# Optimization experiments

Measured on AMD Instinct MI355X. Metric: run time of the kernel, lower is better.

## Reference

```python
import jax, jax.numpy as jnp
import numpy as np
from jax import lax

DIM = 192
D_STATE = 16
D_CONV = 4
EXPAND = 2
DT_RANK = 12  # ceil(192/16)
D_INNER = EXPAND * DIM
MLP_HID = int(DIM * 4.0)
B_, T_, H_, W_ = 2, 8, 24, 24


def _mamba_params(key, prefix):
    ks = jax.random.split(key, 6)
    s = 0.02
    return {
        prefix + "_in_proj_w": jax.random.normal(ks[0], (2 * D_INNER, DIM)) * s,
        prefix + "_conv_w": jax.random.normal(ks[1], (D_INNER, D_CONV)) * s,
        prefix + "_conv_b": jnp.zeros((D_INNER,)),
        prefix + "_x_proj_w": jax.random.normal(ks[2], (DT_RANK + 2 * D_STATE, D_INNER)) * s,
        prefix + "_dt_proj_w": jax.random.normal(ks[3], (D_INNER, DT_RANK)) * s,
        prefix + "_dt_proj_b": jax.random.uniform(ks[4], (D_INNER,), minval=-4.0, maxval=-2.0),
        prefix + "_A_log": jnp.log(jnp.broadcast_to(jnp.arange(1, D_STATE + 1, dtype=jnp.float32), (D_INNER, D_STATE))),
        prefix + "_D": jnp.ones((D_INNER,)),
        prefix + "_out_proj_w": jax.random.normal(ks[5], (DIM, D_INNER)) * s,
    }


def setup_inputs() -> dict:
    key = jax.random.key(0)
    ks = jax.random.split(key, 8)
    s = 0.02
    inp = {"x_in": jax.random.normal(ks[0], (B_, T_, DIM, H_, W_), dtype=jnp.float32)}
    inp["norm1_w"] = jnp.ones((DIM,)); inp["norm1_b"] = jnp.zeros((DIM,))
    inp.update(_mamba_params(ks[1], "s"))
    inp.update(_mamba_params(ks[2], "t"))
    inp["fusion_w"] = jax.random.normal(ks[3], (DIM, 2 * DIM)) * s
    inp["fusion_b"] = jnp.zeros((DIM,))
    inp["norm2_w"] = jnp.ones((DIM,)); inp["norm2_b"] = jnp.zeros((DIM,))
    inp["mlp_w1"] = jax.random.normal(ks[4], (MLP_HID, DIM)) * s
    inp["mlp_b1"] = jnp.zeros((MLP_HID,))
    inp["mlp_w2"] = jax.random.normal(ks[5], (DIM, MLP_HID)) * s
    inp["mlp_b2"] = jnp.zeros((DIM,))
    return inp


def _layer_norm(x, w, b, eps=1e-5):
    m = jnp.mean(x, axis=-1, keepdims=True)
    v = jnp.mean(jnp.square(x - m), axis=-1, keepdims=True)
    return (x - m) * lax.rsqrt(v + eps) * w + b


def _selective_scan(u, delta, A, Bm, Cm, Dp):
    # u, delta: [b,L,d]; A: [d,n]; Bm, Cm: [b,L,n]; Dp: [d]
    dA = jnp.exp(delta[..., None] * A)                       # [b,L,d,n]
    dBu = (delta * u)[..., None] * Bm[:, :, None, :]         # [b,L,d,n]

    def step(h, inp):
        dA_t, dBu_t, C_t = inp                               # [b,d,n],[b,d,n],[b,n]
        h = dA_t * h + dBu_t
        y = jnp.einsum('bdn,bn->bd', h, C_t)
        return h, y

    h0 = jnp.zeros((u.shape[0],) + A.shape, dtype=u.dtype)
    xs = (jnp.moveaxis(dA, 1, 0), jnp.moveaxis(dBu, 1, 0), jnp.moveaxis(Cm, 1, 0))
    _, ys = lax.scan(step, h0, xs)                           # [L,b,d]
    return jnp.moveaxis(ys, 0, 1) + u * Dp


def _mamba(x, in_proj_w, conv_w, conv_b, x_proj_w, dt_proj_w, dt_proj_b, A_log, Dp, out_proj_w):
    # x: [b, L, d_model]
    xz = x @ in_proj_w.T                                     # [b,L,2*d_inner]
    xm, z = jnp.split(xz, 2, axis=-1)
    # causal depthwise conv1d (kernel D_CONV, left-padded)
    xc = jnp.pad(xm, ((0, 0), (D_CONV - 1, 0), (0, 0)))
    kernel = conv_w.T[:, None, :]                            # [W=4, I=1, O=d_inner]
    xm = lax.conv_general_dilated(xc, kernel, (1,), 'VALID',
                                  dimension_numbers=('NWC', 'WIO', 'NWC'),
                                  feature_group_count=D_INNER) + conv_b
    xm = jax.nn.silu(xm)
    dbc = xm @ x_proj_w.T                                    # [b,L,dt_rank+2n]
    dt, Bm, Cm = jnp.split(dbc, [DT_RANK, DT_RANK + D_STATE], axis=-1)
    delta = jax.nn.softplus(dt @ dt_proj_w.T + dt_proj_b)    # [b,L,d_inner]
    A = -jnp.exp(A_log)
    y = _selective_scan(xm, delta, A, Bm, Cm, Dp)
    y = y * jax.nn.silu(z)
    return y @ out_proj_w.T


def reference(x_in, norm1_w, norm1_b,
              s_in_proj_w, s_conv_w, s_conv_b, s_x_proj_w, s_dt_proj_w, s_dt_proj_b, s_A_log, s_D, s_out_proj_w,
              t_in_proj_w, t_conv_w, t_conv_b, t_x_proj_w, t_dt_proj_w, t_dt_proj_b, t_A_log, t_D, t_out_proj_w,
              fusion_w, fusion_b, norm2_w, norm2_b, mlp_w1, mlp_b1, mlp_w2, mlp_b2):
    B, T, C, H, W = x_in.shape
    N = H * W
    x = jnp.transpose(x_in, (0, 1, 3, 4, 2)).reshape(B, T, N, C)
    shortcut = x
    xn = _layer_norm(x, norm1_w, norm1_b)
    out_s = _mamba(xn.reshape(B * T, N, C), s_in_proj_w, s_conv_w, s_conv_b, s_x_proj_w,
                   s_dt_proj_w, s_dt_proj_b, s_A_log, s_D, s_out_proj_w).reshape(B, T, N, C)
    x_t = jnp.transpose(xn, (0, 2, 1, 3)).reshape(B * N, T, C)
    out_t = _mamba(x_t, t_in_proj_w, t_conv_w, t_conv_b, t_x_proj_w,
                   t_dt_proj_w, t_dt_proj_b, t_A_log, t_D, t_out_proj_w)
    out_t = jnp.transpose(out_t.reshape(B, N, T, C), (0, 2, 1, 3))
    fused = jnp.concatenate([out_s, out_t], axis=-1)
    x = shortcut + (fused @ fusion_w.T + fusion_b)
    h = _layer_norm(x, norm2_w, norm2_b)
    h = jax.nn.gelu(h @ mlp_w1.T + mlp_b1, approximate=False) @ mlp_w2.T + mlp_b2
    x = x + h
    return jnp.transpose(x.reshape(B, T, H, W, C), (0, 1, 4, 2, 3))
```

## Files before the change

### kernel.cpp

```cpp
#include <hip/hip_runtime.h>
#include <hip/hip_bf16.h>

#define NB 2
#define NT 8
#define NHW 576
#define NC 192
#define DIN 384
#define NSTATE 16
#define MTOK 9216
#define MLPH 768
#define SCH 36
#define CLEN 16
#define NSEQ_S 16
#define L2E 1.44269504088896f
#define LN2 0.69314718055994f

typedef const __hip_bfloat16* bf16p;
typedef __hip_bfloat16 bf16;

typedef __attribute__((ext_vector_type(8))) short frag_ab;
typedef __attribute__((ext_vector_type(4))) float frag_cd;

__device__ __forceinline__ float b2f(__hip_bfloat16 x) { return __bfloat162float(x); }
__device__ __forceinline__ bf16 f2b(float x) { return __float2bfloat16(x); }

__device__ __forceinline__ bool is_f32(const unsigned* __restrict__ n1w) {
    return n1w[0] == 0x3F800000u;
}

__device__ __forceinline__ float ldv(const void* p, long long i, bool f32) {
    return f32 ? ((const float*)p)[i] : b2f(((const bf16*)p)[i]);
}

__device__ __forceinline__ float siluf(float x) { return x / (1.f + expf(-x)); }
__device__ __forceinline__ float softplus_fast(float x) {
    float e = exp2f(-fabsf(x) * L2E);
    return fmaxf(x, 0.f) + log2f(1.f + e) * LN2;
}
__device__ __forceinline__ float geluf(float x) { return 0.5f * x * (1.f + erff(x * 0.7071067811865476f)); }

__device__ __forceinline__ float wave_sum(float v) {
#pragma unroll
    for (int o = 32; o > 0; o >>= 1) v += __shfl_xor(v, o, 64);
    return v;
}

__global__ __launch_bounds__(256) void ln1_kernel(const void* x_in, const void* w, const void* b,
                                                  bf16* __restrict__ xn,
                                                  bf16* __restrict__ xnt,
                                                  bf16* __restrict__ shortcut,
                                                  const unsigned* __restrict__ n1w) {
    bool f32 = is_f32(n1w);
    int bt = blockIdx.x / 9;
    int hw0 = (blockIdx.x % 9) * 64;
    int bb = bt >> 3, tt = bt & 7;
    int t = threadIdx.x, l = t & 63, wv = t >> 6;
    __shared__ bf16 lv[192 * 66];
    __shared__ float psum[4][64], psq[4][64];
    __shared__ float smean[64], srstd[64];
    __shared__ float swl[192], sbl[192];
    for (int i = t; i < 192; i += 256) { swl[i] = ldv(w, i, f32); sbl[i] = ldv(b, i, f32); }
    float s = 0.f, q = 0.f;
#pragma unroll 4
    for (int cg = 0; cg < 48; cg++) {
        int c = wv * 48 + cg;
        float v = ldv(x_in, (long long)(bt * NC + c) * NHW + hw0 + l, f32);
        lv[c * 66 + l] = f2b(v);
        s += v; q += v * v;
    }
    psum[wv][l] = s; psq[wv][l] = q;
    __syncthreads();
    if (t < 64) {
        float ss = psum[0][t] + psum[1][t] + psum[2][t] + psum[3][t];
        float qq = psq[0][t] + psq[1][t] + psq[2][t] + psq[3][t];
        float mean = ss * (1.f / NC);
        float var = qq * (1.f / NC) - mean * mean;
        smean[t] = mean;
        srstd[t] = rsqrtf(var + 1e-5f);
    }
    __syncthreads();
    for (int jj = 0; jj < 64; jj++) {
        if (t < 192) {
            int n = hw0 + jj;
            long long m = (long long)(bt * NHW + n) * NC + t;
            long long mt = ((long long)(bb * NHW + n) * NT + tt) * NC + t;
            bf16 raw = lv[t * 66 + jj];
            float v = b2f(raw);
            bf16 xv = f2b((v - smean[jj]) * srstd[jj] * swl[t] + sbl[t]);
            shortcut[m] = raw;
            xn[m] = xv;
            xnt[mt] = xv;
        }
    }
}

__global__ __launch_bounds__(64) void ln2_kernel(const float* __restrict__ x, const void* w, const void* b,
                                                 bf16* __restrict__ out,
                                                 const unsigned* __restrict__ n1w) {
    bool f32 = is_f32(n1w);
    int m = blockIdx.x;
    int lane = threadIdx.x;
    float v[3];
#pragma unroll
    for (int r = 0; r < 3; r++) v[r] = x[m * NC + lane + r * 64];
    float s = wave_sum(v[0] + v[1] + v[2]);
    float mean = s * (1.f / NC);
    float q = 0.f;
#pragma unroll
    for (int r = 0; r < 3; r++) { float d = v[r] - mean; q += d * d; }
    q = wave_sum(q);
    float rstd = rsqrtf(q * (1.f / NC) + 1e-5f);
#pragma unroll
    for (int r = 0; r < 3; r++) {
        int c = lane + r * 64;
        out[m * NC + c] = f2b((v[r] - mean) * rstd * ldv(w, c, f32) + ldv(b, c, f32));
    }
}

__device__ __forceinline__ void store_val(float* p, float v) { *p = v; }
__device__ __forceinline__ void store_val(bf16* p, float v) { *p = f2b(v); }
__device__ __forceinline__ float load_val(const float* p) { return *p; }
__device__ __forceinline__ float load_val(const bf16* p) { return b2f(*p); }

__device__ __forceinline__ long long fmode_rowbase(int FMODE, int gm, int N) {
    if (FMODE == 0) return (long long)gm * N;
    if (FMODE == 1) return (long long)gm * 384;
    int b = gm / (NHW * NT);
    int rr = gm % (NHW * NT);
    int n = rr / NT;
    int t = rr % NT;
    int ms = (b * NT + t) * NHW + n;
    return (long long)ms * 384 + 192;
}

#define LDSTR 40
template <int ACT, int FMODE, bool BCHK, typename OutT, typename AddT>
__global__ __launch_bounds__(256) void gemm_mfma(bf16p A, const void* W, const void* bias,
                                                 const AddT* __restrict__ addsrc,
                                                 OutT* __restrict__ out,
                                                 int M, int N, int K,
                                                 const unsigned* __restrict__ n1w) {
    bool f32 = is_f32(n1w);
    __shared__ bf16 lds_a[128 * LDSTR];
    __shared__ bf16 lds_b[64 * LDSTR];
    int tid = threadIdx.x;
    int m0 = blockIdx.y * 128, n0 = blockIdx.x * 64;
    int wv = tid >> 6;
    int lane = tid & 63;
    int lr = lane & 15;
    int quad = lane >> 4;
    int wm = (wv >> 1) * 64;
    int wn = (wv & 1) * 32;

    frag_cd acc[4][2] = {};

    for (int kc = 0; kc < K; kc += 32) {
#pragma unroll
        for (int p = 0; p < 2; p++) {
            int idx = p * 256 + tid;
            int row = idx >> 2;
            int kcol = (idx & 3) * 8;
            *(uint4*)&lds_a[row * LDSTR + kcol] =
                *(const uint4*)&A[(size_t)(m0 + row) * K + kc + kcol];
        }
        {
            int row = tid >> 2;
            int kcol = (tid & 3) * 8;
            bool ok = !BCHK || (n0 + row) < N;
            if (f32) {
                const float* Wf = (const float*)W;
#pragma unroll
                for (int j = 0; j < 8; j++)
                    lds_b[row * LDSTR + kcol + j] =
                        ok ? f2b(Wf[(size_t)(n0 + row) * K + kc + kcol + j]) : f2b(0.f);
            } else {
                uint4 z = {0, 0, 0, 0};
                *(uint4*)&lds_b[row * LDSTR + kcol] =
                    ok ? *(const uint4*)&((const bf16*)W)[(size_t)(n0 + row) * K + kc + kcol] : z;
            }
        }
        __syncthreads();

        frag_ab af[4], bfr[2];
#pragma unroll
        for (int tm = 0; tm < 4; tm++)
            af[tm] = *(const frag_ab*)&lds_a[(wm + tm * 16 + lr) * LDSTR + quad * 8];
#pragma unroll
        for (int tn = 0; tn < 2; tn++)
            bfr[tn] = *(const frag_ab*)&lds_b[(wn + tn * 16 + lr) * LDSTR + quad * 8];
#pragma unroll
        for (int tm = 0; tm < 4; tm++)
#pragma unroll
            for (int tn = 0; tn < 2; tn++)
                acc[tm][tn] = __builtin_amdgcn_mfma_f32_16x16x32_bf16(
                    af[tm], bfr[tn], acc[tm][tn], 0, 0, 0);
        __syncthreads();
    }

#pragma unroll
    for (int tm = 0; tm < 4; tm++) {
#pragma unroll
        for (int r = 0; r < 4; r++) {
            int gm = m0 + wm + tm * 16 + quad * 4 + r;
            long long rowbase = fmode_rowbase(FMODE, gm, N);
#pragma unroll
            for (int tn = 0; tn < 2; tn++) {
                int gn = n0 + wn + tn * 16 + lr;
                if (BCHK && gn >= N) continue;
                float v = acc[tm][tn][r];
                if (bias) v += ldv(bias, gn, f32);
                if (ACT == 1) v = geluf(v);
                if (addsrc) v += load_val(&addsrc[(long long)gm * N + gn]);
                store_val(&out[rowbase + gn], v);
            }
        }
    }
}

template <bool BCHK, int WOFF, typename OutT>
__global__ __launch_bounds__(256) void gemm_dual(bf16p A0, bf16p A1,
                                                 const void* W0, const void* W1,
                                                 OutT* __restrict__ out0,
                                                 OutT* __restrict__ out1,
                                                 int M, int N, int K,
                                                 const unsigned* __restrict__ n1w) {
    bool f32 = is_f32(n1w);
    __shared__ bf16 lds_a[128 * LDSTR];
    __shared__ bf16 lds_b[64 * LDSTR];
    int tid = threadIdx.x;
    bool br0 = blockIdx.y < (unsigned)(M / 128);
    int m0 = (br0 ? blockIdx.y : blockIdx.y - M / 128) * 128;
    int n0 = blockIdx.x * 64;
    bf16p A = br0 ? A0 : A1;
    const void* W = br0 ? W0 : W1;
    OutT* out = br0 ? out0 : out1;
    int wv = tid >> 6;
    int lane = tid & 63;
    int lr = lane & 15;
    int quad = lane >> 4;
    int wm = (wv >> 1) * 64;
    int wn = (wv & 1) * 32;

    frag_cd acc[4][2] = {};

    for (int kc = 0; kc < K; kc += 32) {
#pragma unroll
        for (int p = 0; p < 2; p++) {
            int idx = p * 256 + tid;
            int row = idx >> 2;
            int kcol = (idx & 3) * 8;
            *(uint4*)&lds_a[row * LDSTR + kcol] =
                *(const uint4*)&A[(size_t)(m0 + row) * K + kc + kcol];
        }
        {
            int row = tid >> 2;
            int kcol = (tid & 3) * 8;
            bool ok = !BCHK || (n0 + row) < N;
            size_t wrow = (size_t)(WOFF + n0 + row);
            if (f32) {
                const float* Wf = (const float*)W;
#pragma unroll
                for (int j = 0; j < 8; j++)
                    lds_b[row * LDSTR + kcol + j] =
                        ok ? f2b(Wf[wrow * K + kc + kcol + j]) : f2b(0.f);
            } else {
                uint4 z = {0, 0, 0, 0};
                *(uint4*)&lds_b[row * LDSTR + kcol] =
                    ok ? *(const uint4*)&((const bf16*)W)[wrow * K + kc + kcol] : z;
            }
        }
        __syncthreads();

        frag_ab af[4], bfr[2];
#pragma unroll
        for (int tm = 0; tm < 4; tm++)
            af[tm] = *(const frag_ab*)&lds_a[(wm + tm * 16 + lr) * LDSTR + quad * 8];
#pragma unroll
        for (int tn = 0; tn < 2; tn++)
            bfr[tn] = *(const frag_ab*)&lds_b[(wn + tn * 16 + lr) * LDSTR + quad * 8];
#pragma unroll
        for (int tm = 0; tm < 4; tm++)
#pragma unroll
            for (int tn = 0; tn < 2; tn++)
                acc[tm][tn] = __builtin_amdgcn_mfma_f32_16x16x32_bf16(
                    af[tm], bfr[tn], acc[tm][tn], 0, 0, 0);
        __syncthreads();
    }

#pragma unroll
    for (int tm = 0; tm < 4; tm++) {
#pragma unroll
        for (int r = 0; r < 4; r++) {
            int gm = m0 + wm + tm * 16 + quad * 4 + r;
#pragma unroll
            for (int tn = 0; tn < 2; tn++) {
                int gn = n0 + wn + tn * 16 + lr;
                if (BCHK && gn >= N) continue;
                store_val(&out[(long long)gm * N + gn], acc[tm][tn][r]);
            }
        }
    }
}

__global__ __launch_bounds__(256) void gemm_outproj_dual(bf16p ys_s, bf16p ys_t,
                                                         const void* w_s, const void* w_t,
                                                         bf16* __restrict__ fused,
                                                         const unsigned* __restrict__ n1w) {
    bool f32 = is_f32(n1w);
    __shared__ bf16 lds_a[128 * LDSTR];
    __shared__ bf16 lds_b[64 * LDSTR];
    int tid = threadIdx.x;
    bool spatial = blockIdx.y < (MTOK / 128);
    int m0 = (spatial ? blockIdx.y : blockIdx.y - MTOK / 128) * 128;
    int n0 = blockIdx.x * 64;
    bf16p A = spatial ? ys_s : ys_t;
    const void* W = spatial ? w_s : w_t;
    const int K = DIN;
    int wv = tid >> 6;
    int lane = tid & 63;
    int lr = lane & 15;
    int quad = lane >> 4;
    int wm = (wv >> 1) * 64;
    int wn = (wv & 1) * 32;

    frag_cd acc[4][2] = {};

    for (int kc = 0; kc < K; kc += 32) {
#pragma unroll
        for (int p = 0; p < 2; p++) {
            int idx = p * 256 + tid;
            int row = idx >> 2;
            int kcol = (idx & 3) * 8;
            *(uint4*)&lds_a[row * LDSTR + kcol] =
                *(const uint4*)&A[(size_t)(m0 + row) * K + kc + kcol];
        }
        {
            int row = tid >> 2;
            int kcol = (tid & 3) * 8;
            if (f32) {
                const float* Wf = (const float*)W;
#pragma unroll
                for (int j = 0; j < 8; j++)
                    lds_b[row * LDSTR + kcol + j] =
                        f2b(Wf[(size_t)(n0 + row) * K + kc + kcol + j]);
            } else {
                *(uint4*)&lds_b[row * LDSTR + kcol] =
                    *(const uint4*)&((const bf16*)W)[(size_t)(n0 + row) * K + kc + kcol];
            }
        }
        __syncthreads();

        frag_ab af[4], bfr[2];
#pragma unroll
        for (int tm = 0; tm < 4; tm++)
            af[tm] = *(const frag_ab*)&lds_a[(wm + tm * 16 + lr) * LDSTR + quad * 8];
#pragma unroll
        for (int tn = 0; tn < 2; tn++)
            bfr[tn] = *(const frag_ab*)&lds_b[(wn + tn * 16 + lr) * LDSTR + quad * 8];
#pragma unroll
        for (int tm = 0; tm < 4; tm++)
#pragma unroll
            for (int tn = 0; tn < 2; tn++)
                acc[tm][tn] = __builtin_amdgcn_mfma_f32_16x16x32_bf16(
                    af[tm], bfr[tn], acc[tm][tn], 0, 0, 0);
        __syncthreads();
    }

#pragma unroll
    for (int tm = 0; tm < 4; tm++) {
#pragma unroll
        for (int r = 0; r < 4; r++) {
            int gm = m0 + wm + tm * 16 + quad * 4 + r;
            long long rowbase = fmode_rowbase(spatial ? 1 : 2, gm, NC);
#pragma unroll
            for (int tn = 0; tn < 2; tn++) {
                int gn = n0 + wn + tn * 16 + lr;
                fused[rowbase + gn] = f2b(acc[tm][tn][r]);
            }
        }
    }
}

#define TOTEL (MTOK * DIN)
__global__ __launch_bounds__(256) void conv_dual(bf16p xs, const void* cw_s, const void* cb_s,
                                                 bf16p xt, const void* cw_t, const void* cb_t,
                                                 bf16* __restrict__ xm_s,
                                                 bf16* __restrict__ xm_t,
                                                 const unsigned* __restrict__ n1w) {
    bool f32 = is_f32(n1w);
    long long gidx = (long long)blockIdx.x * blockDim.x + threadIdx.x;
    bool sp = gidx < TOTEL;
    long long idx = sp ? gidx : gidx - TOTEL;
    bf16p x = sp ? xs : xt;
    const void* cw = sp ? cw_s : cw_t;
    const void* cb = sp ? cb_s : cb_t;
    bf16* xm = sp ? xm_s : xm_t;
    int L = sp ? NHW : NT;
    int d = (int)(idx % DIN);
    long long rem = idx / DIN;
    int l = (int)(rem % L);
    long long seq = rem / L;
    float s = ldv(cb, d, f32);
#pragma unroll
    for (int k = 0; k < 4; k++) {
        int ll = l - 3 + k;
        if (ll >= 0) s += ldv(cw, d * 4 + k, f32) * b2f(x[(seq * L + ll) * DIN + d]);
    }
    xm[(seq * L + l) * DIN + d] = f2b(siluf(s));
}

template <int TL>
__global__ __launch_bounds__(128) void scan_kernel(bf16p xm,
                                                   const float* __restrict__ dbc,
                                                   bf16* __restrict__ zy,
                                                   const void* dtw, const void* dtb,
                                                   const void* A_log, const void* Dv,
                                                   const unsigned* __restrict__ n1w) {
    bool f32 = is_f32(n1w);
    int seq = blockIdx.x / 3;
    int d = (blockIdx.x % 3) * 128 + threadIdx.x;
    int row0 = seq * TL;
    __shared__ float sdbc[TL * 44];
    for (int i = threadIdx.x; i < TL * 44; i += 128)
        sdbc[i] = dbc[(long long)row0 * 44 + i];
    bf16 um[TL], zm[TL];
#pragma unroll
    for (int t = 0; t < TL; t++) {
        um[t] = xm[(long long)(row0 + t) * DIN + d];
        zm[t] = zy[(long long)(row0 + t) * DIN + d];
    }
    float A2[NSTATE], h[NSTATE];
#pragma unroll
    for (int n = 0; n < NSTATE; n++) {
        A2[n] = -expf(ldv(A_log, d * NSTATE + n, f32)) * L2E;
        h[n] = 0.f;
    }
    float wdt[12];
#pragma unroll
    for (int r = 0; r < 12; r++) wdt[r] = ldv(dtw, d * 12 + r, f32);
    float bdt = ldv(dtb, d, f32);
    float Dd = ldv(Dv, d, f32);
    __syncthreads();
#pragma unroll
    for (int t = 0; t < TL; t++) {
        const float* dr = &sdbc[t * 44];
        float s = bdt;
#pragma unroll
        for (int r = 0; r < 12; r++) s += dr[r] * wdt[r];
        float dv = softplus_fast(s);
        float uv = b2f(um[t]);
        float du = dv * uv;
        float y = 0.f;
#pragma unroll
        for (int n = 0; n < NSTATE; n++) {
            float dA = exp2f(dv * A2[n]);
            h[n] = h[n] * dA + du * dr[12 + n];
            y += h[n] * dr[28 + n];
        }
        y += uv * Dd;
        zy[(long long)(row0 + t) * DIN + d] = f2b(y * siluf(b2f(zm[t])));
    }
}

__global__ __launch_bounds__(256) void scan1_kernel(bf16p xm,
                                                    const float* __restrict__ dbc,
                                                    const void* dtw, const void* dtb,
                                                    const void* A_log,
                                                    bf16* __restrict__ hfin,
                                                    float* __restrict__ dsumb,
                                                    const unsigned* __restrict__ n1w) {
    bool f32 = is_f32(n1w);
    int bid = blockIdx.x;
    int part = bid % 3;
    int ch = (bid / 3) % SCH;
    int seq = bid / (3 * SCH);
    int tid = threadIdx.x;
    int wave = tid >> 6;
    int lane = tid & 63;
    int dl = lane & 31;
    int nh = lane >> 5;
    int d = part * 128 + wave * 32 + dl;
    int nbase = nh * 8;
    int row0 = seq * NHW + ch * CLEN;
    __shared__ float sdbc[CLEN * 44];
    for (int i = tid; i < CLEN * 44; i += 256)
        sdbc[i] = dbc[(long long)row0 * 44 + i];
    bf16 um[CLEN];
#pragma unroll
    for (int t = 0; t < CLEN; t++)
        um[t] = xm[(long long)(row0 + t) * DIN + d];
    float A2[8], h[8];
#pragma unroll
    for (int j = 0; j < 8; j++) {
        A2[j] = -expf(ldv(A_log, d * NSTATE + nbase + j, f32)) * L2E;
        h[j] = 0.f;
    }
    float wdt[12];
#pragma unroll
    for (int r = 0; r < 12; r++) wdt[r] = ldv(dtw, d * 12 + r, f32);
    float bdt = ldv(dtb, d, f32);
    float dsum = 0.f;
    __syncthreads();
#pragma unroll
    for (int t = 0; t < CLEN; t++) {
        const float* dr = &sdbc[t * 44];
        float s = bdt;
#pragma unroll
        for (int r = 0; r < 12; r++) s += dr[r] * wdt[r];
        float dv = softplus_fast(s);
        dsum += dv;
        float du = dv * b2f(um[t]);
#pragma unroll
        for (int j = 0; j < 8; j++) {
            float dA = exp2f(dv * A2[j]);
            h[j] = h[j] * dA + du * dr[12 + nbase + j];
        }
    }
    long long base = (((long long)seq * SCH + ch) * DIN + d) * NSTATE + nbase;
#pragma unroll
    for (int j = 0; j < 8; j++) hfin[base + j] = f2b(h[j]);
    if (nh == 0) dsumb[((long long)seq * SCH + ch) * DIN + d] = dsum;
}

__global__ __launch_bounds__(256) void scan2_kernel(bf16* __restrict__ hfin,
                                                    const float* __restrict__ dsumb,
                                                    const void* A_log,
                                                    const unsigned* __restrict__ n1w) {
    bool f32 = is_f32(n1w);
    int e = blockIdx.x * blockDim.x + threadIdx.x;
    int seq = e / (DIN * NSTATE);
    int dn = e % (DIN * NSTATE);
    int d = dn >> 4;
    float A2 = -expf(ldv(A_log, dn, f32)) * L2E;
    float hrun = 0.f;
    for (int ch = 0; ch < SCH; ch++) {
        long long cidx = (long long)seq * SCH + ch;
        float p = exp2f(dsumb[cidx * DIN + d] * A2);
        long long idx = cidx * (DIN * NSTATE) + dn;
        float hf = b2f(hfin[idx]);
        hfin[idx] = f2b(hrun);
        hrun = p * hrun + hf;
    }
}

__global__ __launch_bounds__(256) void scan3_kernel(bf16p xm,
                                                    const float* __restrict__ dbc,
                                                    bf16* __restrict__ zy,
                                                    const void* dtw, const void* dtb,
                                                    const void* A_log, const void* Dv,
                                                    const bf16* __restrict__ hinit,
                                                    const unsigned* __restrict__ n1w) {
    bool f32 = is_f32(n1w);
    int bid = blockIdx.x;
    int part = bid % 3;
    int ch = (bid / 3) % SCH;
    int seq = bid / (3 * SCH);
    int tid = threadIdx.x;
    int wave = tid >> 6;
    int lane = tid & 63;
    int dl = lane & 31;
    int nh = lane >> 5;
    int d = part * 128 + wave * 32 + dl;
    int nbase = nh * 8;
    int row0 = seq * NHW + ch * CLEN;
    __shared__ float sdbc[CLEN * 44];
    for (int i = tid; i < CLEN * 44; i += 256)
        sdbc[i] = dbc[(long long)row0 * 44 + i];
    bf16 um[CLEN], zm[CLEN];
#pragma unroll
    for (int t = 0; t < CLEN; t++) {
        um[t] = xm[(long long)(row0 + t) * DIN + d];
        zm[t] = zy[(long long)(row0 + t) * DIN + d];
    }
    long long base = (((long long)seq * SCH + ch) * DIN + d) * NSTATE + nbase;
    float A2[8], h[8];
#pragma unroll
    for (int j = 0; j < 8; j++) {
        A2[j] = -expf(ldv(A_log, d * NSTATE + nbase + j, f32)) * L2E;
        h[j] = b2f(hinit[base + j]);
    }
    float wdt[12];
#pragma unroll
    for (int r = 0; r < 12; r++) wdt[r] = ldv(dtw, d * 12 + r, f32);
    float bdt = ldv(dtb, d, f32);
    float Dd = ldv(Dv, d, f32);
    __syncthreads();
#pragma unroll
    for (int t = 0; t < CLEN; t++) {
        const float* dr = &sdbc[t * 44];
        float s = bdt;
#pragma unroll
        for (int r = 0; r < 12; r++) s += dr[r] * wdt[r];
        float dv = softplus_fast(s);
        float uv = b2f(um[t]);
        float du = dv * uv;
        float y = 0.f;
#pragma unroll
        for (int j = 0; j < 8; j++) {
            float dA = exp2f(dv * A2[j]);
            h[j] = h[j] * dA + du * dr[12 + nbase + j];
            y += h[j] * dr[28 + nbase + j];
        }
        y += __shfl_xor(y, 32, 64);
        if (nh == 0) {
            y += uv * Dd;
            zy[(long long)(row0 + t) * DIN + d] = f2b(y * siluf(b2f(zm[t])));
        }
    }
}

__global__ __launch_bounds__(256) void out_kernel(const float* __restrict__ fin,
                                                  void* __restrict__ out,
                                                  const unsigned* __restrict__ n1w) {
    bool f32 = is_f32(n1w);
    int bt = blockIdx.x / 9;
    int hw0 = (blockIdx.x % 9) * 64;
    int t = threadIdx.x, l = t & 63, wv = t >> 6;
    __shared__ float lf[192 * 67];
    for (int jj = 0; jj < 64; jj++) {
        if (t < 192)
            lf[t * 67 + jj] = fin[(long long)(bt * NHW + hw0 + jj) * NC + t];
    }
    __syncthreads();
#pragma unroll 4
    for (int cg = 0; cg < 48; cg++) {
        int c = wv * 48 + cg;
        float v = lf[c * 67 + l];
        long long o = (long long)(bt * NC + c) * NHW + hw0 + l;
        if (f32) ((float*)out)[o] = v;
        else     ((bf16*)out)[o] = f2b(v);
    }
}

extern "C" void kernel_launch(void* const* d_in, const int* in_sizes, int n_in,
                              void* d_out, int out_size, void* d_ws, size_t ws_size,
                              hipStream_t stream) {
    const void* x_in   = d_in[0];
    const unsigned* n1w = (const unsigned*)d_in[1];
    const void* n1b    = d_in[2];
    const void* s_inw  = d_in[3];
    const void* s_cw   = d_in[4];
    const void* s_cb   = d_in[5];
    const void* s_xw   = d_in[6];
    const void* s_dtw  = d_in[7];
    const void* s_dtb  = d_in[8];
    const void* s_alog = d_in[9];
    const void* s_d    = d_in[10];
    const void* s_ow   = d_in[11];
    const void* t_inw  = d_in[12];
    const void* t_cw   = d_in[13];
    const void* t_cb   = d_in[14];
    const void* t_xw   = d_in[15];
    const void* t_dtw  = d_in[16];
    const void* t_dtb  = d_in[17];
    const void* t_alog = d_in[18];
    const void* t_d    = d_in[19];
    const void* t_ow   = d_in[20];
    const void* fw     = d_in[21];
    const void* fb     = d_in[22];
    const void* n2w    = d_in[23];
    const void* n2b    = d_in[24];
    const void* w1     = d_in[25];
    const void* b1     = d_in[26];
    const void* w2     = d_in[27];
    const void* b2     = d_in[28];

    char* p = (char*)d_ws;
    p += 16;
    bf16* XN    = (bf16*)p; p += (size_t)MTOK * NC * 2;
    bf16* SHORT = (bf16*)p; p += (size_t)MTOK * NC * 2;
    bf16* XNT   = (bf16*)p; p += (size_t)MTOK * NC * 2;
    bf16* S3    = (bf16*)p; p += (size_t)MTOK * 384 * 2;
    bf16* S4A   = (bf16*)p; p += (size_t)MTOK * DIN * 2;
    bf16* S4B   = (bf16*)p; p += (size_t)MTOK * DIN * 2;
    bf16* S5    = (bf16*)p; p += (size_t)MTOK * DIN * 2;
    bf16* S6    = (bf16*)p; p += (size_t)MTOK * DIN * 2;
    float* DBCS = (float*)p; p += (size_t)MTOK * 44 * 4;
    float* S8   = (float*)p; p += (size_t)MTOK * NC * 4;
    bf16*  HFIN  = S3;
    bf16*  FUSED = S3;
    bf16*  XMS   = S5;
    bf16*  XMT   = S6;
    float* FINAL = (float*)S5;
    bf16*  H     = S6;
    bf16*  HMID  = S4A;
    float* DBCT  = S8;
    float* DSUM  = S8 + (size_t)MTOK * 44;
    float* X2    = S8;

    ln1_kernel<<<144, 256, 0, stream>>>(x_in, n1w, n1b, XN, XNT, SHORT, n1w);

    gemm_dual<false, 0, bf16><<<dim3(DIN / 64, 2 * MTOK / 128), 256, 0, stream>>>(
        XN, XNT, s_inw, t_inw, S4A, S4B, MTOK, DIN, NC, n1w);

    conv_dual<<<(unsigned)((2LL * TOTEL + 255) / 256), 256, 0, stream>>>(
        S4A, s_cw, s_cb, S4B, t_cw, t_cb, XMS, XMT, n1w);

    gemm_dual<true, 0, float><<<dim3(1, 2 * MTOK / 128), 256, 0, stream>>>(
        XMS, XMT, s_xw, t_xw, DBCS, DBCT, MTOK, 44, DIN, n1w);

    gemm_dual<false, 384, bf16><<<dim3(DIN / 64, 2 * MTOK / 128), 256, 0, stream>>>(
        XN, XNT, s_inw, t_inw, S4A, S4B, MTOK, DIN, NC, n1w);

    scan1_kernel<<<NSEQ_S * SCH * 3, 256, 0, stream>>>(XMS, DBCS, s_dtw, s_dtb, s_alog, HFIN, DSUM, n1w);
    scan2_kernel<<<NSEQ_S * DIN * NSTATE / 256, 256, 0, stream>>>(HFIN, DSUM, s_alog, n1w);
    scan3_kernel<<<NSEQ_S * SCH * 3, 256, 0, stream>>>(XMS, DBCS, S4A, s_dtw, s_dtb, s_alog, s_d, HFIN, n1w);

    scan_kernel<NT><<<NB * NHW * 3, 128, 0, stream>>>(XMT, DBCT, S4B, t_dtw, t_dtb, t_alog, t_d, n1w);

    gemm_outproj_dual<<<dim3(NC / 64, 2 * MTOK / 128), 256, 0, stream>>>(S4A, S4B, s_ow, t_ow, FUSED, n1w);

    gemm_mfma<0, 0, false, float, bf16><<<dim3(NC / 64, MTOK / 128), 256, 0, stream>>>(FUSED, fw, fb, SHORT, X2, MTOK, NC, 2 * NC, n1w);

    ln2_kernel<<<MTOK, 64, 0, stream>>>(X2, n2w, n2b, H, n1w);
    gemm_mfma<1, 0, false, bf16, float><<<dim3(MLPH / 64, MTOK / 128), 256, 0, stream>>>(H, w1, b1, nullptr, HMID, MTOK, MLPH, NC, n1w);
    gemm_mfma<0, 0, false, float, float><<<dim3(NC / 64, MTOK / 128), 256, 0, stream>>>(HMID, w2, b2, X2, FINAL, MTOK, NC, MLPH, n1w);

    out_kernel<<<144, 256, 0, stream>>>(FINAL, d_out, n1w);
}
```

Baseline: 442.9 us.

## Merge x_proj and z-projection GEMMs, and spatial scan1 with temporal scan

Merges the x_proj GEMM and the z-half in_proj GEMM into one launch that dispatches on block index. It also merges the spatial chunk scan (phase 1) with the full temporal scan into one launch, packing two temporal sequences per 256-thread block. The aim is to cut kernel launch overhead and let independent work fill the GPU together instead of running in sequence. The cost is divergent block roles with different register use, so occupancy is set by the heavier branch.

```diff
diff --git a/kernel.cpp b/kernel.cpp
--- a/kernel.cpp
+++ b/kernel.cpp
@@ -302,6 +302,149 @@
     }
 }
 
+__global__ __launch_bounds__(256) void xproj_z_kernel(
+    bf16p xms, bf16p xmt, const void* xw_s, const void* xw_t,
+    float* __restrict__ dbcs, float* __restrict__ dbct,
+    bf16p xn, bf16p xnt, const void* inw_s, const void* inw_t,
+    bf16* __restrict__ zs, bf16* __restrict__ zt,
+    const unsigned* __restrict__ n1w) {
+    bool f32 = is_f32(n1w);
+    __shared__ bf16 lds_a[128 * LDSTR];
+    __shared__ bf16 lds_b[64 * LDSTR];
+    int tid = threadIdx.x;
+    int wv = tid >> 6;
+    int lane = tid & 63;
+    int lr = lane & 15;
+    int quad = lane >> 4;
+    int wm = (wv >> 1) * 64;
+    int wn = (wv & 1) * 32;
+    frag_cd acc[4][2] = {};
+
+    if (blockIdx.x < 144) {
+        bool br0 = blockIdx.x < 72;
+        int m0 = (br0 ? blockIdx.x : blockIdx.x - 72) * 128;
+        bf16p A = br0 ? xms : xmt;
+        const void* W = br0 ? xw_s : xw_t;
+        float* out = br0 ? dbcs : dbct;
+        const int N = 44, K = DIN;
+        for (int kc = 0; kc < K; kc += 32) {
+#pragma unroll
+            for (int p = 0; p < 2; p++) {
+                int idx = p * 256 + tid;
+                int row = idx >> 2;
+                int kcol = (idx & 3) * 8;
+                *(uint4*)&lds_a[row * LDSTR + kcol] =
+                    *(const uint4*)&A[(size_t)(m0 + row) * K + kc + kcol];
+            }
+            {
+                int row = tid >> 2;
+                int kcol = (tid & 3) * 8;
+                bool ok = row < N;
+                if (f32) {
+                    const float* Wf = (const float*)W;
+#pragma unroll
+                    for (int j = 0; j < 8; j++)
+                        lds_b[row * LDSTR + kcol + j] =
+                            ok ? f2b(Wf[(size_t)row * K + kc + kcol + j]) : f2b(0.f);
+                } else {
+                    uint4 z = {0, 0, 0, 0};
+                    *(uint4*)&lds_b[row * LDSTR + kcol] =
+                        ok ? *(const uint4*)&((const bf16*)W)[(size_t)row * K + kc + kcol] : z;
+                }
+            }
+            __syncthreads();
+            frag_ab af[4], bfr[2];
+#pragma unroll
+            for (int tm = 0; tm < 4; tm++)
+                af[tm] = *(const frag_ab*)&lds_a[(wm + tm * 16 + lr) * LDSTR + quad * 8];
+#pragma unroll
+            for (int tn = 0; tn < 2; tn++)
+                bfr[tn] = *(const frag_ab*)&lds_b[(wn + tn * 16 + lr) * LDSTR + quad * 8];
+#pragma unroll
+            for (int tm = 0; tm < 4; tm++)
+#pragma unroll
+                for (int tn = 0; tn < 2; tn++)
+                    acc[tm][tn] = __builtin_amdgcn_mfma_f32_16x16x32_bf16(
+                        af[tm], bfr[tn], acc[tm][tn], 0, 0, 0);
+            __syncthreads();
+        }
+#pragma unroll
+        for (int tm = 0; tm < 4; tm++) {
+#pragma unroll
+            for (int r = 0; r < 4; r++) {
+                int gm = m0 + wm + tm * 16 + quad * 4 + r;
+#pragma unroll
+                for (int tn = 0; tn < 2; tn++) {
+                    int gn = wn + tn * 16 + lr;
+                    if (gn >= N) continue;
+                    out[(long long)gm * N + gn] = acc[tm][tn][r];
+                }
+            }
+        }
+    } else {
+        int rel = blockIdx.x - 144;
+        bool br0 = rel < 432;
+        int r2 = br0 ? rel : rel - 432;
+        int n0 = (r2 % 6) * 64;
+        int m0 = (r2 / 6) * 128;
+        bf16p A = br0 ? xn : xnt;
+        const void* W = br0 ? inw_s : inw_t;
+        bf16* out = br0 ? zs : zt;
+        const int N = DIN, K = NC;
+        for (int kc = 0; kc < K; kc += 32) {
+#pragma unroll
+            for (int p = 0; p < 2; p++) {
+                int idx = p * 256 + tid;
+                int row = idx >> 2;
+                int kcol = (idx & 3) * 8;
+                *(uint4*)&lds_a[row * LDSTR + kcol] =
+                    *(const uint4*)&A[(size_t)(m0 + row) * K + kc + kcol];
+            }
+            {
+                int row = tid >> 2;
+                int kcol = (tid & 3) * 8;
+                size_t wrow = (size_t)(384 + n0 + row);
+                if (f32) {
+                    const float* Wf = (const float*)W;
+#pragma unroll
+                    for (int j = 0; j < 8; j++)
+                        lds_b[row * LDSTR + kcol + j] = f2b(Wf[wrow * K + kc + kcol + j]);
+                } else {
+                    *(uint4*)&lds_b[row * LDSTR + kcol] =
+                        *(const uint4*)&((const bf16*)W)[wrow * K + kc + kcol];
+                }
+            }
+            __syncthreads();
+            frag_ab af[4], bfr[2];
+#pragma unroll
+            for (int tm = 0; tm < 4; tm++)
+                af[tm] = *(const frag_ab*)&lds_a[(wm + tm * 16 + lr) * LDSTR + quad * 8];
+#pragma unroll
+            for (int tn = 0; tn < 2; tn++)
+                bfr[tn] = *(const frag_ab*)&lds_b[(wn + tn * 16 + lr) * LDSTR + quad * 8];
+#pragma unroll
+            for (int tm = 0; tm < 4; tm++)
+#pragma unroll
+                for (int tn = 0; tn < 2; tn++)
+                    acc[tm][tn] = __builtin_amdgcn_mfma_f32_16x16x32_bf16(
+                        af[tm], bfr[tn], acc[tm][tn], 0, 0, 0);
+            __syncthreads();
+        }
+#pragma unroll
+        for (int tm = 0; tm < 4; tm++) {
+#pragma unroll
+            for (int r = 0; r < 4; r++) {
+                int gm = m0 + wm + tm * 16 + quad * 4 + r;
+#pragma unroll
+                for (int tn = 0; tn < 2; tn++) {
+                    int gn = n0 + wn + tn * 16 + lr;
+                    out[(long long)gm * N + gn] = f2b(acc[tm][tn][r]);
+                }
+            }
+        }
+    }
+}
+
 __global__ __launch_bounds__(256) void gemm_outproj_dual(bf16p ys_s, bf16p ys_t,
                                                          const void* w_s, const void* w_t,
                                                          bf16* __restrict__ fused,
@@ -409,117 +552,115 @@
     xm[(seq * L + l) * DIN + d] = f2b(siluf(s));
 }
 
-template <int TL>
-__global__ __launch_bounds__(128) void scan_kernel(bf16p xm,
-                                                   const float* __restrict__ dbc,
-                                                   bf16* __restrict__ zy,
-                                                   const void* dtw, const void* dtb,
-                                                   const void* A_log, const void* Dv,
-                                                   const unsigned* __restrict__ n1w) {
-    bool f32 = is_f32(n1w);
-    int seq = blockIdx.x / 3;
-    int d = (blockIdx.x % 3) * 128 + threadIdx.x;
-    int row0 = seq * TL;
-    __shared__ float sdbc[TL * 44];
-    for (int i = threadIdx.x; i < TL * 44; i += 128)
-        sdbc[i] = dbc[(long long)row0 * 44 + i];
-    bf16 um[TL], zm[TL];
-#pragma unroll
-    for (int t = 0; t < TL; t++) {
-        um[t] = xm[(long long)(row0 + t) * DIN + d];
-        zm[t] = zy[(long long)(row0 + t) * DIN + d];
-    }
-    float A2[NSTATE], h[NSTATE];
-#pragma unroll
-    for (int n = 0; n < NSTATE; n++) {
-        A2[n] = -expf(ldv(A_log, d * NSTATE + n, f32)) * L2E;
-        h[n] = 0.f;
-    }
-    float wdt[12];
-#pragma unroll
-    for (int r = 0; r < 12; r++) wdt[r] = ldv(dtw, d * 12 + r, f32);
-    float bdt = ldv(dtb, d, f32);
-    float Dd = ldv(Dv, d, f32);
-    __syncthreads();
-#pragma unroll
-    for (int t = 0; t < TL; t++) {
-        const float* dr = &sdbc[t * 44];
-        float s = bdt;
-#pragma unroll
-        for (int r = 0; r < 12; r++) s += dr[r] * wdt[r];
-        float dv = softplus_fast(s);
-        float uv = b2f(um[t]);
-        float du = dv * uv;
-        float y = 0.f;
+__global__ __launch_bounds__(256) void scan_front_kernel(
+    bf16p xms, const float* __restrict__ dbcs,
+    const void* s_dtw, const void* s_dtb, const void* s_alog,
+    bf16* __restrict__ hfin, float* __restrict__ dsumb,
+    bf16p xmt, const float* __restrict__ dbct, bf16* __restrict__ zyt,
+    const void* t_dtw, const void* t_dtb, const void* t_alog, const void* t_dv,
+    const unsigned* __restrict__ n1w) {
+    bool f32 = is_f32(n1w);
+    __shared__ float sdbc[704];
+    int tid = threadIdx.x;
+
+    if (blockIdx.x < 1728) {
+        int bid = blockIdx.x;
+        int part = bid % 3;
+        int ch = (bid / 3) % SCH;
+        int seq = bid / (3 * SCH);
+        int wave = tid >> 6;
+        int lane = tid & 63;
+        int dl = lane & 31;
+        int nh = lane >> 5;
+        int d = part * 128 + wave * 32 + dl;
+        int nbase = nh * 8;
+        int row0 = seq * NHW + ch * CLEN;
+        for (int i = tid; i < CLEN * 44; i += 256)
+            sdbc[i] = dbcs[(long long)row0 * 44 + i];
+        bf16 um[CLEN];
+#pragma unroll
+        for (int t = 0; t < CLEN; t++)
+            um[t] = xms[(long long)(row0 + t) * DIN + d];
+        float A2[8], h[8];
+#pragma unroll
+        for (int j = 0; j < 8; j++) {
+            A2[j] = -expf(ldv(s_alog, d * NSTATE + nbase + j, f32)) * L2E;
+            h[j] = 0.f;
+        }
+        float wdt[12];
+#pragma unroll
+        for (int r = 0; r < 12; r++) wdt[r] = ldv(s_dtw, d * 12 + r, f32);
+        float bdt = ldv(s_dtb, d, f32);
+        float dsum = 0.f;
+        __syncthreads();
+#pragma unroll
+        for (int t = 0; t < CLEN; t++) {
+            const float* dr = &sdbc[t * 44];
+            float s = bdt;
+#pragma unroll
+            for (int r = 0; r < 12; r++) s += dr[r] * wdt[r];
+            float dv = softplus_fast(s);
+            dsum += dv;
+            float du = dv * b2f(um[t]);
+#pragma unroll
+            for (int j = 0; j < 8; j++) {
+                float dA = exp2f(dv * A2[j]);
+                h[j] = h[j] * dA + du * dr[12 + nbase + j];
+            }
+        }
+        long long base = (((long long)seq * SCH + ch) * DIN + d) * NSTATE + nbase;
+#pragma unroll
+        for (int j = 0; j < 8; j++) hfin[base + j] = f2b(h[j]);
+        if (nh == 0) dsumb[((long long)seq * SCH + ch) * DIN + d] = dsum;
+    } else {
+        int rel = blockIdx.x - 1728;
+        int sub = tid >> 7;
+        int ltid = tid & 127;
+        int orig = rel * 2 + sub;
+        int seq = orig / 3;
+        int d = (orig % 3) * 128 + ltid;
+        int row0 = seq * NT;
+        float* my_dbc = &sdbc[sub * 352];
+        for (int i = ltid; i < NT * 44; i += 128)
+            my_dbc[i] = dbct[(long long)row0 * 44 + i];
+        bf16 um[NT], zm[NT];
+#pragma unroll
+        for (int t = 0; t < NT; t++) {
+            um[t] = xmt[(long long)(row0 + t) * DIN + d];
+            zm[t] = zyt[(long long)(row0 + t) * DIN + d];
+        }
+        float A2[NSTATE], h[NSTATE];
 #pragma unroll
         for (int n = 0; n < NSTATE; n++) {
-            float dA = exp2f(dv * A2[n]);
-            h[n] = h[n] * dA + du * dr[12 + n];
-            y += h[n] * dr[28 + n];
-        }
-        y += uv * Dd;
-        zy[(long long)(row0 + t) * DIN + d] = f2b(y * siluf(b2f(zm[t])));
-    }
-}
-
-__global__ __launch_bounds__(256) void scan1_kernel(bf16p xm,
-                                                    const float* __restrict__ dbc,
-                                                    const void* dtw, const void* dtb,
-                                                    const void* A_log,
-                                                    bf16* __restrict__ hfin,
-                                                    float* __restrict__ dsumb,
-                                                    const unsigned* __restrict__ n1w) {
-    bool f32 = is_f32(n1w);
-    int bid = blockIdx.x;
-    int part = bid % 3;
-    int ch = (bid / 3) % SCH;
-    int seq = bid / (3 * SCH);
-    int tid = threadIdx.x;
-    int wave = tid >> 6;
-    int lane = tid & 63;
-    int dl = lane & 31;
-    int nh = lane >> 5;
-    int d = part * 128 + wave * 32 + dl;
-    int nbase = nh * 8;
-    int row0 = seq * NHW + ch * CLEN;
-    __shared__ float sdbc[CLEN * 44];
-    for (int i = tid; i < CLEN * 44; i += 256)
-        sdbc[i] = dbc[(long long)row0 * 44 + i];
-    bf16 um[CLEN];
-#pragma unroll
-    for (int t = 0; t < CLEN; t++)
-        um[t] = xm[(long long)(row0 + t) * DIN + d];
-    float A2[8], h[8];
-#pragma unroll
-    for (int j = 0; j < 8; j++) {
-        A2[j] = -expf(ldv(A_log, d * NSTATE + nbase + j, f32)) * L2E;
-        h[j] = 0.f;
-    }
-    float wdt[12];
-#pragma unroll
-    for (int r = 0; r < 12; r++) wdt[r] = ldv(dtw, d * 12 + r, f32);
-    float bdt = ldv(dtb, d, f32);
-    float dsum = 0.f;
-    __syncthreads();
-#pragma unroll
-    for (int t = 0; t < CLEN; t++) {
-        const float* dr = &sdbc[t * 44];
-        float s = bdt;
-#pragma unroll
-        for (int r = 0; r < 12; r++) s += dr[r] * wdt[r];
-        float dv = softplus_fast(s);
-        dsum += dv;
-        float du = dv * b2f(um[t]);
-#pragma unroll
-        for (int j = 0; j < 8; j++) {
-            float dA = exp2f(dv * A2[j]);
-            h[j] = h[j] * dA + du * dr[12 + nbase + j];
-        }
-    }
-    long long base = (((long long)seq * SCH + ch) * DIN + d) * NSTATE + nbase;
-#pragma unroll
-    for (int j = 0; j < 8; j++) hfin[base + j] = f2b(h[j]);
-    if (nh == 0) dsumb[((long long)seq * SCH + ch) * DIN + d] = dsum;
+            A2[n] = -expf(ldv(t_alog, d * NSTATE + n, f32)) * L2E;
+            h[n] = 0.f;
+        }
+        float wdt[12];
+#pragma unroll
+        for (int r = 0; r < 12; r++) wdt[r] = ldv(t_dtw, d * 12 + r, f32);
+        float bdt = ldv(t_dtb, d, f32);
+        float Dd = ldv(t_dv, d, f32);
+        __syncthreads();
+#pragma unroll
+        for (int t = 0; t < NT; t++) {
+            const float* dr = &my_dbc[t * 44];
+            float s = bdt;
+#pragma unroll
+            for (int r = 0; r < 12; r++) s += dr[r] * wdt[r];
+            float dv = softplus_fast(s);
+            float uv = b2f(um[t]);
+            float du = dv * uv;
+            float y = 0.f;
+#pragma unroll
+            for (int n = 0; n < NSTATE; n++) {
+                float dA = exp2f(dv * A2[n]);
+                h[n] = h[n] * dA + du * dr[12 + n];
+                y += h[n] * dr[28 + n];
+            }
+            y += uv * Dd;
+            zyt[(long long)(row0 + t) * DIN + d] = f2b(y * siluf(b2f(zm[t])));
+        }
+    }
 }
 
 __global__ __launch_bounds__(256) void scan2_kernel(bf16* __restrict__ hfin,
@@ -696,17 +837,16 @@
     conv_dual<<<(unsigned)((2LL * TOTEL + 255) / 256), 256, 0, stream>>>(
         S4A, s_cw, s_cb, S4B, t_cw, t_cb, XMS, XMT, n1w);
 
-    gemm_dual<true, 0, float><<<dim3(1, 2 * MTOK / 128), 256, 0, stream>>>(
-        XMS, XMT, s_xw, t_xw, DBCS, DBCT, MTOK, 44, DIN, n1w);
-
-    gemm_dual<false, 384, bf16><<<dim3(DIN / 64, 2 * MTOK / 128), 256, 0, stream>>>(
-        XN, XNT, s_inw, t_inw, S4A, S4B, MTOK, DIN, NC, n1w);
-
-    scan1_kernel<<<NSEQ_S * SCH * 3, 256, 0, stream>>>(XMS, DBCS, s_dtw, s_dtb, s_alog, HFIN, DSUM, n1w);
+    xproj_z_kernel<<<1008, 256, 0, stream>>>(
+        XMS, XMT, s_xw, t_xw, DBCS, DBCT,
+        XN, XNT, s_inw, t_inw, S4A, S4B, n1w);
+
+    scan_front_kernel<<<3456, 256, 0, stream>>>(
+        XMS, DBCS, s_dtw, s_dtb, s_alog, HFIN, DSUM,
+        XMT, DBCT, S4B, t_dtw, t_dtb, t_alog, t_d, n1w);
+
     scan2_kernel<<<NSEQ_S * DIN * NSTATE / 256, 256, 0, stream>>>(HFIN, DSUM, s_alog, n1w);
     scan3_kernel<<<NSEQ_S * SCH * 3, 256, 0, stream>>>(XMS, DBCS, S4A, s_dtw, s_dtb, s_alog, s_d, HFIN, n1w);
-
-    scan_kernel<NT><<<NB * NHW * 3, 128, 0, stream>>>(XMT, DBCT, S4B, t_dtw, t_dtb, t_alog, t_d, n1w);
 
     gemm_outproj_dual<<<dim3(NC / 64, 2 * MTOK / 128), 256, 0, stream>>>(S4A, S4B, s_ow, t_ow, FUSED, n1w);
 
```

Measured after the change: 432.1 us. 2.4% less time.
